# Kernel tuning notes

Measured on AMD Instinct MI355X. Metric: run time of the kernel, lower is better.

Reference implementation:

```python
import jax, jax.numpy as jnp
import numpy as np

N, M, D = 32768, 2048, 32


def setup_inputs() -> dict:
    key = jax.random.key(0)
    k1, k2, k3, k4 = jax.random.split(key, 4)
    inputs = jax.random.normal(k1, (N, D), dtype=jnp.float32)
    # matches torch init: abs(10*randn*0.1 + 0.2)
    gamma = jnp.abs(10.0 * jax.random.normal(k2, (M, D, D), dtype=jnp.float32) * 0.1 + 0.2)
    means = jax.random.normal(k3, (M, D), dtype=jnp.float32)
    weights = jax.random.normal(k4, (M,), dtype=jnp.float32)
    return {"inputs": inputs, "gamma": gamma, "means": means, "weights": weights}


def reference(inputs, gamma, means, weights):
    # cov_m = gamma_m @ gamma_m^T  -> symmetric PSD [M, D, D]
    cov = jnp.einsum('mde,mfe->mdf', gamma, gamma)
    # Quadratic form (x - mu)^T C (x - mu) expanded (C symmetric):
    # x^T C_m x via GEMM on flattened outer products: [N, D*D] @ [D*D, M]
    xx = (inputs[:, :, None] * inputs[:, None, :]).reshape(inputs.shape[0], -1)
    quad_x = xx @ cov.reshape(cov.shape[0], -1).T            # [N, M]
    b = jnp.einsum('mde,me->md', cov, means)                 # C_m mu_m, [M, D]
    cross = inputs @ b.T                                     # x^T C_m mu_m, [N, M]
    const = jnp.einsum('md,md->m', b, means)                 # mu^T C mu, [M]
    D_ij = quad_x - 2.0 * cross + const[None, :]             # [N, M]
    out = jnp.exp(-D_ij) @ weights                           # [N]
    return out[:, None]
```

## Files before the change

### kernel.cpp

```cpp
#include <hip/hip_runtime.h>
#include <math.h>


#define NN 32768
#define MM 2048
#define DDIM 32
#define KSYM 576
#define ROWS 128
#define KSTEPS 18
#define SCREEN 120.0f
#define MCAP 2048
#define FCAP 1000000
#define FBLK 64

typedef __attribute__((ext_vector_type(8))) short short8;
typedef __attribute__((ext_vector_type(4))) float floatx4;

__device__ __forceinline__ unsigned int to_bf16(float f) {
  union { float f; unsigned int u; } x; x.f = f;
  return (x.u + 0x7fffu + ((x.u >> 16) & 1u)) >> 16;
}

struct DFTab { unsigned char d[528]; unsigned char f[528]; };
constexpr DFTab make_df() {
  DFTab t{};
  int s = 0;
  for (int d = 0; d < 32; ++d)
    for (int f = d; f < 32; ++f) {
      t.d[s] = (unsigned char)d; t.f[s] = (unsigned char)f; ++s;
    }
  return t;
}
constexpr DFTab DFT = make_df();

__device__ __forceinline__ float slot_val(const float* v, int s) {
  if (s < 528) return v[DFT.d[s]] * v[DFT.f[s]];
  if (s < 560) return v[s - 528];
  if (s < 562) return 1.f;
  return 0.f;
}

__device__ __forceinline__ void slot_df(int s, int* dd, int* ff) {
  int d = 0, b = 0;
  while (b + (DDIM - d) <= s) { b += DDIM - d; ++d; }
  *dd = d; *ff = d + (s - b);
}

__global__ __launch_bounds__(256) void build_b_kernel(
    const float* __restrict__ gamma, const float* __restrict__ means,
    unsigned short* __restrict__ Bm) {
  __shared__ float G[DDIM][DDIM + 1];
  __shared__ float C[DDIM][DDIM + 1];
  __shared__ float bv[DDIM];
  __shared__ float cc;
  const int m = blockIdx.x;
  const int t = threadIdx.x;
  const float* g = gamma + (size_t)m * DDIM * DDIM;
  for (int l = t; l < DDIM * DDIM; l += 256) G[l >> 5][l & 31] = g[l];
  __syncthreads();
  const float* mu = means + m * DDIM;
  for (int l = t; l < DDIM * DDIM; l += 256) {
    int d = l >> 5, f = l & 31;
    float c = 0.f;
#pragma unroll
    for (int e = 0; e < DDIM; ++e) c += G[d][e] * G[f][e];
    C[d][f] = c;
  }
  __syncthreads();
  if (t < DDIM) {
    float b = 0.f;
#pragma unroll
    for (int f = 0; f < DDIM; ++f) b += C[t][f] * mu[f];
    bv[t] = b;
  }
  __syncthreads();
  if (t == 0) {
    float c = 0.f;
#pragma unroll
    for (int d = 0; d < DDIM; ++d) c += bv[d] * mu[d];
    cc = c;
  }
  __syncthreads();
  unsigned short* brow = Bm + (size_t)m * KSYM;
  for (int s = t; s < KSYM; s += 256) {
    float val;
    if (s < 528) {
      int d, f; slot_df(s, &d, &f);
      val = (d == f) ? C[d][d] : 2.f * C[d][f];
    } else if (s < 560) {
      val = -2.f * bv[s - 528];
    } else if (s == 560) {
      val = cc;
    } else if (s == 561) {
      unsigned int hi = to_bf16(cc);
      union { unsigned int u; float f; } xh; xh.u = hi << 16;
      val = cc - xh.f;
    } else {
      val = 0.f;
    }
    brow[s] = (unsigned short)to_bf16(val);
  }
}

__device__ __noinline__ double survivor_contrib(
    int m, const float* __restrict__ gamma, const float* __restrict__ means,
    const float* __restrict__ weights, const float* __restrict__ xrow) {
  const float* mu = means + m * DDIM;
  float v[DDIM];
#pragma unroll
  for (int d = 0; d < DDIM; ++d) v[d] = xrow[d] - mu[d];
  const float* g = gamma + (size_t)m * DDIM * DDIM;
  float Dex = 0.f;
  for (int e = 0; e < DDIM; ++e) {
    float y = 0.f;
#pragma unroll
    for (int d = 0; d < DDIM; ++d) y += g[d * DDIM + e] * v[d];
    Dex += y * y;
  }
  float e2 = -Dex * 1.44269504088896340736f;
  float kf = floorf(e2);
  float mant = exp2f(e2 - kf);
  return ldexp((double)(weights[m] * mant), (int)kf);
}

__global__ __launch_bounds__(512, 1) void screen_kernel(
    const float* __restrict__ x, const unsigned short* __restrict__ Bm,
    unsigned int* __restrict__ mcnt, unsigned short* __restrict__ mlist,
    unsigned int* __restrict__ flist, unsigned int* __restrict__ fcount) {
  extern __shared__ __align__(16) unsigned short As[];
  const int t = threadIdx.x;
  const int i0 = blockIdx.x * ROWS;
  const int lane = t & 63, w = t >> 6;
  const int lrow = lane & 15, quad = lane >> 4;
  const int rot = blockIdx.x & 31;

  {
    const int r = t >> 2, j = t & 3;
    float v[DDIM];
#pragma unroll
    for (int q = 0; q < 8; ++q)
      *(floatx4*)&v[q * 4] = *(const floatx4*)(x + (size_t)(i0 + r) * DDIM + q * 4);
#pragma unroll
    for (int jj = 0; jj < 4; ++jj) {
      if (j == jj) {
#pragma unroll
        for (int cc = 0; cc < 18; ++cc) {
          const int c = jj * 18 + cc;
          unsigned int uu[4];
#pragma unroll
          for (int q = 0; q < 4; ++q) {
            const int s0 = c * 8 + q * 2;
            uu[q] = to_bf16(slot_val(v, s0)) | (to_bf16(slot_val(v, s0 + 1)) << 16);
          }
          const int cs = (c & ~7) | ((c & 7) ^ (r & 7));
          uint4 o; o.x = uu[0]; o.y = uu[1]; o.z = uu[2]; o.w = uu[3];
          *(uint4*)&As[r * KSYM + cs * 8] = o;
        }
      }
    }
  }
  __syncthreads();

#pragma unroll 1
  for (int g = 0; g < 4; ++g) {
    const int mq = ((g * 8 + w) + rot) & 31;
    const int m0 = mq * 64;
    const unsigned short* bb0 = Bm + (size_t)(m0 +  0 + lrow) * KSYM + quad * 8;
    const unsigned short* bb1 = Bm + (size_t)(m0 + 16 + lrow) * KSYM + quad * 8;
    const unsigned short* bb2 = Bm + (size_t)(m0 + 32 + lrow) * KSYM + quad * 8;
    const unsigned short* bb3 = Bm + (size_t)(m0 + 48 + lrow) * KSYM + quad * 8;

    floatx4 acc[8][4] = {};
#pragma unroll
    for (int kk = 0; kk < KSTEPS; ++kk) {
      short8 bf[4];
      bf[0] = *(const short8*)(bb0 + kk * 32);
      bf[1] = *(const short8*)(bb1 + kk * 32);
      bf[2] = *(const short8*)(bb2 + kk * 32);
      bf[3] = *(const short8*)(bb3 + kk * 32);
      short8 af[8];
#pragma unroll
      for (int ti = 0; ti < 8; ++ti) {
        int rr = ti * 16 + lrow;
        int c = kk * 4 + quad;
        int cs = (c & ~7) | ((c & 7) ^ (rr & 7));
        af[ti] = *(const short8*)&As[rr * KSYM + cs * 8];
      }
#pragma unroll
      for (int ti = 0; ti < 8; ++ti)
#pragma unroll
        for (int mj = 0; mj < 4; ++mj)
          acc[ti][mj] = __builtin_amdgcn_mfma_f32_16x16x32_bf16(
              af[ti], bf[mj], acc[ti][mj], 0, 0, 0);
    }

#pragma unroll
    for (int ti = 0; ti < 8; ++ti)
#pragma unroll
      for (int mj = 0; mj < 4; ++mj)
#pragma unroll
        for (int r = 0; r < 4; ++r) {
          float Dt = acc[ti][mj][r];
          if (Dt < SCREEN) {
            int gi = i0 + ti * 16 + quad * 4 + r;
            int gm = m0 + mj * 16 + lrow;
            unsigned int idx = atomicAdd(&mcnt[gm], 1u);
            if (idx < MCAP) {
              mlist[(size_t)gm * MCAP + idx] = (unsigned short)gi;
            } else {
              unsigned int fi = atomicAdd(fcount, 1u);
              if (fi < FCAP)
                flist[fi] = ((unsigned int)gi << 11) | (unsigned int)gm;
            }
          }
        }
  }
}

__global__ __launch_bounds__(256) void survivor2_kernel(
    const unsigned int* __restrict__ mcnt, const unsigned short* __restrict__ mlist,
    const unsigned int* __restrict__ flist, const unsigned int* __restrict__ fcount,
    const float* __restrict__ x, const float* __restrict__ gamma,
    const float* __restrict__ means, const float* __restrict__ weights,
    double* __restrict__ acc_out) {
  const int blk = blockIdx.x;
  const int t = threadIdx.x;
  if (blk >= MM) {
    unsigned int total = *fcount;
    if (total > FCAP) total = FCAP;
    for (unsigned int idx = (blk - MM) * 256 + t; idx < total; idx += FBLK * 256) {
      unsigned int p = flist[idx];
      int gi = (int)(p >> 11), gm = (int)(p & 2047u);
      double c = survivor_contrib(gm, gamma, means, weights, x + (size_t)gi * DDIM);
      atomicAdd(&acc_out[gi], c);
    }
    return;
  }
  __shared__ float Gt[DDIM][DDIM + 1];
  __shared__ float mu[DDIM];
  const int m = blk;
  unsigned int cnt = mcnt[m];
  if (cnt > MCAP) cnt = MCAP;
  if (cnt == 0) return;
  const float* g = gamma + (size_t)m * DDIM * DDIM;
  for (int l = t; l < DDIM * DDIM; l += 256) Gt[l & 31][l >> 5] = g[l];
  if (t < DDIM) mu[t] = means[m * DDIM + t];
  __syncthreads();
  const float wm = weights[m];
  for (unsigned int s = t; s < cnt; s += 256) {
    int gi = mlist[(size_t)m * MCAP + s];
    float v[DDIM];
#pragma unroll
    for (int q = 0; q < 8; ++q) {
      floatx4 xv = *(const floatx4*)(x + (size_t)gi * DDIM + q * 4);
      v[q * 4 + 0] = xv.x - mu[q * 4 + 0];
      v[q * 4 + 1] = xv.y - mu[q * 4 + 1];
      v[q * 4 + 2] = xv.z - mu[q * 4 + 2];
      v[q * 4 + 3] = xv.w - mu[q * 4 + 3];
    }
    float Dex = 0.f;
#pragma unroll
    for (int e = 0; e < DDIM; ++e) {
      float y = 0.f;
#pragma unroll
      for (int d = 0; d < DDIM; ++d) y += Gt[e][d] * v[d];
      Dex += y * y;
    }
    float e2 = -Dex * 1.44269504088896340736f;
    float kf = floorf(e2);
    float mant = exp2f(e2 - kf);
    atomicAdd(&acc_out[gi], ldexp((double)(wm * mant), (int)kf));
  }
}

__global__ __launch_bounds__(256) void finalize_kernel(
    const double* __restrict__ acc, float* __restrict__ out) {
  int i = blockIdx.x * 256 + threadIdx.x;
  out[i] = (float)acc[i];
}

extern "C" void kernel_launch(void* const* d_in, const int* in_sizes, int n_in,
                              void* d_out, int out_size, void* d_ws, size_t ws_size,
                              hipStream_t stream) {
  (void)in_sizes; (void)n_in; (void)out_size;
  const float* x       = (const float*)d_in[0];
  const float* gamma   = (const float*)d_in[1];
  const float* means   = (const float*)d_in[2];
  const float* weights = (const float*)d_in[3];

  char* p = (char*)d_ws;
  double* acc          = (double*)p;            p += (size_t)NN * 8;
  unsigned int* fcount = (unsigned int*)p;      p += 16;
  unsigned int* mcnt   = (unsigned int*)p;      p += (size_t)MM * 4;
  unsigned short* mlist= (unsigned short*)p;    p += (size_t)MM * MCAP * 2;
  unsigned int* flist  = (unsigned int*)p;      p += (size_t)FCAP * 4;
  unsigned short* Bm   = (unsigned short*)p;    p += (size_t)MM * KSYM * 2;
  const size_t needed = (size_t)(p - (char*)d_ws);
  const size_t zero_bytes = (size_t)NN * 8 + 16 + (size_t)MM * 4;
  if (ws_size < needed) return;

  (void)hipFuncSetAttribute((const void*)screen_kernel,
                            hipFuncAttributeMaxDynamicSharedMemorySize,
                            ROWS * KSYM * 2);

  hipMemsetAsync(d_ws, 0, zero_bytes, stream);
  hipLaunchKernelGGL(build_b_kernel, dim3(MM), dim3(256), 0, stream, gamma, means, Bm);
  hipLaunchKernelGGL(screen_kernel, dim3(NN / ROWS), dim3(512),
                     ROWS * KSYM * 2, stream,
                     x, Bm, mcnt, mlist, flist, fcount);
  hipLaunchKernelGGL(survivor2_kernel, dim3(MM + FBLK), dim3(256), 0, stream,
                     mcnt, mlist, flist, fcount, x, gamma, means, weights, acc);
  hipLaunchKernelGGL(finalize_kernel, dim3(NN / 256), dim3(256), 0, stream,
                     acc, (float*)d_out);
}
```

Measured before the change: 185.1 us.

## Fuse build, screen, survivor and finalize into one cooperative persistent kernel

```diff
diff --git a/kernel.cpp b/kernel.cpp
--- a/kernel.cpp
+++ b/kernel.cpp
@@ -1,5 +1,8 @@
 #include <hip/hip_runtime.h>
+#include <hip/hip_cooperative_groups.h>
 #include <math.h>
+
+namespace cg = cooperative_groups;
 
 
 #define NN 32768
@@ -11,7 +14,8 @@
 #define SCREEN 120.0f
 #define MCAP 2048
 #define FCAP 1000000
-#define FBLK 64
+#define GRID 256
+#define TPB 512
 
 typedef __attribute__((ext_vector_type(8))) short short8;
 typedef __attribute__((ext_vector_type(4))) float floatx4;
@@ -46,62 +50,6 @@
   *dd = d; *ff = d + (s - b);
 }
 
-__global__ __launch_bounds__(256) void build_b_kernel(
-    const float* __restrict__ gamma, const float* __restrict__ means,
-    unsigned short* __restrict__ Bm) {
-  __shared__ float G[DDIM][DDIM + 1];
-  __shared__ float C[DDIM][DDIM + 1];
-  __shared__ float bv[DDIM];
-  __shared__ float cc;
-  const int m = blockIdx.x;
-  const int t = threadIdx.x;
-  const float* g = gamma + (size_t)m * DDIM * DDIM;
-  for (int l = t; l < DDIM * DDIM; l += 256) G[l >> 5][l & 31] = g[l];
-  __syncthreads();
-  const float* mu = means + m * DDIM;
-  for (int l = t; l < DDIM * DDIM; l += 256) {
-    int d = l >> 5, f = l & 31;
-    float c = 0.f;
-#pragma unroll
-    for (int e = 0; e < DDIM; ++e) c += G[d][e] * G[f][e];
-    C[d][f] = c;
-  }
-  __syncthreads();
-  if (t < DDIM) {
-    float b = 0.f;
-#pragma unroll
-    for (int f = 0; f < DDIM; ++f) b += C[t][f] * mu[f];
-    bv[t] = b;
-  }
-  __syncthreads();
-  if (t == 0) {
-    float c = 0.f;
-#pragma unroll
-    for (int d = 0; d < DDIM; ++d) c += bv[d] * mu[d];
-    cc = c;
-  }
-  __syncthreads();
-  unsigned short* brow = Bm + (size_t)m * KSYM;
-  for (int s = t; s < KSYM; s += 256) {
-    float val;
-    if (s < 528) {
-      int d, f; slot_df(s, &d, &f);
-      val = (d == f) ? C[d][d] : 2.f * C[d][f];
-    } else if (s < 560) {
-      val = -2.f * bv[s - 528];
-    } else if (s == 560) {
-      val = cc;
-    } else if (s == 561) {
-      unsigned int hi = to_bf16(cc);
-      union { unsigned int u; float f; } xh; xh.u = hi << 16;
-      val = cc - xh.f;
-    } else {
-      val = 0.f;
-    }
-    brow[s] = (unsigned short)to_bf16(val);
-  }
-}
-
 __device__ __noinline__ double survivor_contrib(
     int m, const float* __restrict__ gamma, const float* __restrict__ means,
     const float* __restrict__ weights, const float* __restrict__ xrow) {
@@ -123,160 +71,232 @@
   return ldexp((double)(weights[m] * mant), (int)kf);
 }
 
-__global__ __launch_bounds__(512, 1) void screen_kernel(
-    const float* __restrict__ x, const unsigned short* __restrict__ Bm,
-    unsigned int* __restrict__ mcnt, unsigned short* __restrict__ mlist,
-    unsigned int* __restrict__ flist, unsigned int* __restrict__ fcount) {
+__global__ __launch_bounds__(TPB, 1) void fused_kernel(
+    const float* __restrict__ x, const float* __restrict__ gamma,
+    const float* __restrict__ means, const float* __restrict__ weights,
+    unsigned short* __restrict__ Bm, unsigned int* __restrict__ mcnt,
+    unsigned short* __restrict__ mlist, unsigned int* __restrict__ flist,
+    unsigned int* __restrict__ fcount, double* __restrict__ acc_g,
+    float* __restrict__ out) {
   extern __shared__ __align__(16) unsigned short As[];
+  cg::grid_group grid = cg::this_grid();
   const int t = threadIdx.x;
-  const int i0 = blockIdx.x * ROWS;
-  const int lane = t & 63, w = t >> 6;
-  const int lrow = lane & 15, quad = lane >> 4;
-  const int rot = blockIdx.x & 31;
+  const int blk = blockIdx.x;
 
   {
-    const int r = t >> 2, j = t & 3;
-    float v[DDIM];
-#pragma unroll
-    for (int q = 0; q < 8; ++q)
-      *(floatx4*)&v[q * 4] = *(const floatx4*)(x + (size_t)(i0 + r) * DDIM + q * 4);
-#pragma unroll
-    for (int jj = 0; jj < 4; ++jj) {
-      if (j == jj) {
-#pragma unroll
-        for (int cc = 0; cc < 18; ++cc) {
-          const int c = jj * 18 + cc;
-          unsigned int uu[4];
-#pragma unroll
-          for (int q = 0; q < 4; ++q) {
-            const int s0 = c * 8 + q * 2;
-            uu[q] = to_bf16(slot_val(v, s0)) | (to_bf16(slot_val(v, s0 + 1)) << 16);
+    if (t < 128) acc_g[blk * 128 + t] = 0.0;
+    if (t >= 128 && t < 136) mcnt[blk * 8 + (t - 128)] = 0u;
+    if (blk == 0 && t == 136) *fcount = 0u;
+  }
+
+  {
+    float* G  = (float*)As;
+    float* C  = G + 32 * 33;
+    float* bv = C + 32 * 33;
+    float* cp = bv + 32;
+#pragma unroll 1
+    for (int mi = 0; mi < 8; ++mi) {
+      const int m = blk * 8 + mi;
+      const float* g = gamma + (size_t)m * DDIM * DDIM;
+      const float* mu = means + m * DDIM;
+      for (int l = t; l < DDIM * DDIM; l += TPB) G[(l >> 5) * 33 + (l & 31)] = g[l];
+      __syncthreads();
+      for (int l = t; l < DDIM * DDIM; l += TPB) {
+        int d = l >> 5, f = l & 31;
+        float c = 0.f;
+#pragma unroll
+        for (int e = 0; e < DDIM; ++e) c += G[d * 33 + e] * G[f * 33 + e];
+        C[d * 33 + f] = c;
+      }
+      __syncthreads();
+      if (t < DDIM) {
+        float b = 0.f;
+#pragma unroll
+        for (int f = 0; f < DDIM; ++f) b += C[t * 33 + f] * mu[f];
+        bv[t] = b;
+      }
+      __syncthreads();
+      if (t == 0) {
+        float c = 0.f;
+#pragma unroll
+        for (int d = 0; d < DDIM; ++d) c += bv[d] * mu[d];
+        *cp = c;
+      }
+      __syncthreads();
+      unsigned short* brow = Bm + (size_t)m * KSYM;
+      const float cc = *cp;
+      for (int s = t; s < KSYM; s += TPB) {
+        float val;
+        if (s < 528) {
+          int d, f; slot_df(s, &d, &f);
+          val = (d == f) ? C[d * 33 + d] : 2.f * C[d * 33 + f];
+        } else if (s < 560) {
+          val = -2.f * bv[s - 528];
+        } else if (s == 560) {
+          val = cc;
+        } else if (s == 561) {
+          unsigned int hi = to_bf16(cc);
+          union { unsigned int u; float f; } xh; xh.u = hi << 16;
+          val = cc - xh.f;
+        } else {
+          val = 0.f;
+        }
+        brow[s] = (unsigned short)to_bf16(val);
+      }
+      __syncthreads();
+    }
+  }
+
+  grid.sync();
+
+  {
+    const int i0 = blk * ROWS;
+    const int lane = t & 63, w = t >> 6;
+    const int lrow = lane & 15, quad = lane >> 4;
+    const int rot = blk & 31;
+
+    {
+      const int r = t >> 2, j = t & 3;
+      float v[DDIM];
+#pragma unroll
+      for (int q = 0; q < 8; ++q)
+        *(floatx4*)&v[q * 4] = *(const floatx4*)(x + (size_t)(i0 + r) * DDIM + q * 4);
+#pragma unroll
+      for (int jj = 0; jj < 4; ++jj) {
+        if (j == jj) {
+#pragma unroll
+          for (int cc2 = 0; cc2 < 18; ++cc2) {
+            const int c = jj * 18 + cc2;
+            unsigned int uu[4];
+#pragma unroll
+            for (int q = 0; q < 4; ++q) {
+              const int s0 = c * 8 + q * 2;
+              uu[q] = to_bf16(slot_val(v, s0)) | (to_bf16(slot_val(v, s0 + 1)) << 16);
+            }
+            const int cs = (c & ~7) | ((c & 7) ^ (r & 7));
+            uint4 o; o.x = uu[0]; o.y = uu[1]; o.z = uu[2]; o.w = uu[3];
+            *(uint4*)&As[r * KSYM + cs * 8] = o;
           }
-          const int cs = (c & ~7) | ((c & 7) ^ (r & 7));
-          uint4 o; o.x = uu[0]; o.y = uu[1]; o.z = uu[2]; o.w = uu[3];
-          *(uint4*)&As[r * KSYM + cs * 8] = o;
         }
       }
     }
-  }
-  __syncthreads();
+    __syncthreads();
 
 #pragma unroll 1
-  for (int g = 0; g < 4; ++g) {
-    const int mq = ((g * 8 + w) + rot) & 31;
-    const int m0 = mq * 64;
-    const unsigned short* bb0 = Bm + (size_t)(m0 +  0 + lrow) * KSYM + quad * 8;
-    const unsigned short* bb1 = Bm + (size_t)(m0 + 16 + lrow) * KSYM + quad * 8;
-    const unsigned short* bb2 = Bm + (size_t)(m0 + 32 + lrow) * KSYM + quad * 8;
-    const unsigned short* bb3 = Bm + (size_t)(m0 + 48 + lrow) * KSYM + quad * 8;
-
-    floatx4 acc[8][4] = {};
-#pragma unroll
-    for (int kk = 0; kk < KSTEPS; ++kk) {
-      short8 bf[4];
-      bf[0] = *(const short8*)(bb0 + kk * 32);
-      bf[1] = *(const short8*)(bb1 + kk * 32);
-      bf[2] = *(const short8*)(bb2 + kk * 32);
-      bf[3] = *(const short8*)(bb3 + kk * 32);
-      short8 af[8];
-#pragma unroll
-      for (int ti = 0; ti < 8; ++ti) {
-        int rr = ti * 16 + lrow;
-        int c = kk * 4 + quad;
-        int cs = (c & ~7) | ((c & 7) ^ (rr & 7));
-        af[ti] = *(const short8*)&As[rr * KSYM + cs * 8];
-      }
+    for (int g = 0; g < 4; ++g) {
+      const int mq = ((g * 8 + w) + rot) & 31;
+      const int m0 = mq * 64;
+      const unsigned short* bb0 = Bm + (size_t)(m0 +  0 + lrow) * KSYM + quad * 8;
+      const unsigned short* bb1 = Bm + (size_t)(m0 + 16 + lrow) * KSYM + quad * 8;
+      const unsigned short* bb2 = Bm + (size_t)(m0 + 32 + lrow) * KSYM + quad * 8;
+      const unsigned short* bb3 = Bm + (size_t)(m0 + 48 + lrow) * KSYM + quad * 8;
+
+      floatx4 acc[8][4] = {};
+#pragma unroll
+      for (int kk = 0; kk < KSTEPS; ++kk) {
+        short8 bf[4];
+        bf[0] = *(const short8*)(bb0 + kk * 32);
+        bf[1] = *(const short8*)(bb1 + kk * 32);
+        bf[2] = *(const short8*)(bb2 + kk * 32);
+        bf[3] = *(const short8*)(bb3 + kk * 32);
+        short8 af[8];
+#pragma unroll
+        for (int ti = 0; ti < 8; ++ti) {
+          int rr = ti * 16 + lrow;
+          int c = kk * 4 + quad;
+          int cs = (c & ~7) | ((c & 7) ^ (rr & 7));
+          af[ti] = *(const short8*)&As[rr * KSYM + cs * 8];
+        }
+#pragma unroll
+        for (int ti = 0; ti < 8; ++ti)
+#pragma unroll
+          for (int mj = 0; mj < 4; ++mj)
+            acc[ti][mj] = __builtin_amdgcn_mfma_f32_16x16x32_bf16(
+                af[ti], bf[mj], acc[ti][mj], 0, 0, 0);
+      }
+
 #pragma unroll
       for (int ti = 0; ti < 8; ++ti)
 #pragma unroll
         for (int mj = 0; mj < 4; ++mj)
-          acc[ti][mj] = __builtin_amdgcn_mfma_f32_16x16x32_bf16(
-              af[ti], bf[mj], acc[ti][mj], 0, 0, 0);
-    }
-
-#pragma unroll
-    for (int ti = 0; ti < 8; ++ti)
-#pragma unroll
-      for (int mj = 0; mj < 4; ++mj)
-#pragma unroll
-        for (int r = 0; r < 4; ++r) {
-          float Dt = acc[ti][mj][r];
-          if (Dt < SCREEN) {
-            int gi = i0 + ti * 16 + quad * 4 + r;
-            int gm = m0 + mj * 16 + lrow;
-            unsigned int idx = atomicAdd(&mcnt[gm], 1u);
-            if (idx < MCAP) {
-              mlist[(size_t)gm * MCAP + idx] = (unsigned short)gi;
-            } else {
-              unsigned int fi = atomicAdd(fcount, 1u);
-              if (fi < FCAP)
-                flist[fi] = ((unsigned int)gi << 11) | (unsigned int)gm;
+#pragma unroll
+          for (int r = 0; r < 4; ++r) {
+            float Dt = acc[ti][mj][r];
+            if (Dt < SCREEN) {
+              int gi = i0 + ti * 16 + quad * 4 + r;
+              int gm = m0 + mj * 16 + lrow;
+              unsigned int idx = atomicAdd(&mcnt[gm], 1u);
+              if (idx < MCAP) {
+                mlist[(size_t)gm * MCAP + idx] = (unsigned short)gi;
+              } else {
+                unsigned int fi = atomicAdd(fcount, 1u);
+                if (fi < FCAP)
+                  flist[fi] = ((unsigned int)gi << 11) | (unsigned int)gm;
+              }
             }
           }
+    }
+  }
+
+  grid.sync();
+
+  {
+    float* Gt = (float*)As;
+    float* mus = Gt + 32 * 33;
+#pragma unroll 1
+    for (int mi = 0; mi < 8; ++mi) {
+      const int m = blk * 8 + mi;
+      unsigned int cnt = mcnt[m];
+      if (cnt > MCAP) cnt = MCAP;
+      if (cnt > 0) {
+        const float* g = gamma + (size_t)m * DDIM * DDIM;
+        for (int l = t; l < DDIM * DDIM; l += TPB) Gt[(l & 31) * 33 + (l >> 5)] = g[l];
+        if (t < DDIM) mus[t] = means[m * DDIM + t];
+        __syncthreads();
+        const float wm = weights[m];
+        for (unsigned int s = t; s < cnt; s += TPB) {
+          int gi = mlist[(size_t)m * MCAP + s];
+          float v[DDIM];
+#pragma unroll
+          for (int q = 0; q < 8; ++q) {
+            floatx4 xv = *(const floatx4*)(x + (size_t)gi * DDIM + q * 4);
+            v[q * 4 + 0] = xv.x - mus[q * 4 + 0];
+            v[q * 4 + 1] = xv.y - mus[q * 4 + 1];
+            v[q * 4 + 2] = xv.z - mus[q * 4 + 2];
+            v[q * 4 + 3] = xv.w - mus[q * 4 + 3];
+          }
+          float Dex = 0.f;
+#pragma unroll
+          for (int e = 0; e < DDIM; ++e) {
+            float y = 0.f;
+#pragma unroll
+            for (int d = 0; d < DDIM; ++d) y += Gt[e * 33 + d] * v[d];
+            Dex += y * y;
+          }
+          float e2 = -Dex * 1.44269504088896340736f;
+          float kf = floorf(e2);
+          float mant = exp2f(e2 - kf);
+          atomicAdd(&acc_g[gi], ldexp((double)(wm * mant), (int)kf));
         }
-  }
-}
-
-__global__ __launch_bounds__(256) void survivor2_kernel(
-    const unsigned int* __restrict__ mcnt, const unsigned short* __restrict__ mlist,
-    const unsigned int* __restrict__ flist, const unsigned int* __restrict__ fcount,
-    const float* __restrict__ x, const float* __restrict__ gamma,
-    const float* __restrict__ means, const float* __restrict__ weights,
-    double* __restrict__ acc_out) {
-  const int blk = blockIdx.x;
-  const int t = threadIdx.x;
-  if (blk >= MM) {
+        __syncthreads();
+      }
+    }
     unsigned int total = *fcount;
     if (total > FCAP) total = FCAP;
-    for (unsigned int idx = (blk - MM) * 256 + t; idx < total; idx += FBLK * 256) {
-      unsigned int p = flist[idx];
-      int gi = (int)(p >> 11), gm = (int)(p & 2047u);
+    for (unsigned int idx = blk * TPB + t; idx < total; idx += GRID * TPB) {
+      unsigned int pck = flist[idx];
+      int gi = (int)(pck >> 11), gm = (int)(pck & 2047u);
       double c = survivor_contrib(gm, gamma, means, weights, x + (size_t)gi * DDIM);
-      atomicAdd(&acc_out[gi], c);
-    }
-    return;
-  }
-  __shared__ float Gt[DDIM][DDIM + 1];
-  __shared__ float mu[DDIM];
-  const int m = blk;
-  unsigned int cnt = mcnt[m];
-  if (cnt > MCAP) cnt = MCAP;
-  if (cnt == 0) return;
-  const float* g = gamma + (size_t)m * DDIM * DDIM;
-  for (int l = t; l < DDIM * DDIM; l += 256) Gt[l & 31][l >> 5] = g[l];
-  if (t < DDIM) mu[t] = means[m * DDIM + t];
-  __syncthreads();
-  const float wm = weights[m];
-  for (unsigned int s = t; s < cnt; s += 256) {
-    int gi = mlist[(size_t)m * MCAP + s];
-    float v[DDIM];
-#pragma unroll
-    for (int q = 0; q < 8; ++q) {
-      floatx4 xv = *(const floatx4*)(x + (size_t)gi * DDIM + q * 4);
-      v[q * 4 + 0] = xv.x - mu[q * 4 + 0];
-      v[q * 4 + 1] = xv.y - mu[q * 4 + 1];
-      v[q * 4 + 2] = xv.z - mu[q * 4 + 2];
-      v[q * 4 + 3] = xv.w - mu[q * 4 + 3];
-    }
-    float Dex = 0.f;
-#pragma unroll
-    for (int e = 0; e < DDIM; ++e) {
-      float y = 0.f;
-#pragma unroll
-      for (int d = 0; d < DDIM; ++d) y += Gt[e][d] * v[d];
-      Dex += y * y;
-    }
-    float e2 = -Dex * 1.44269504088896340736f;
-    float kf = floorf(e2);
-    float mant = exp2f(e2 - kf);
-    atomicAdd(&acc_out[gi], ldexp((double)(wm * mant), (int)kf));
-  }
-}
-
-__global__ __launch_bounds__(256) void finalize_kernel(
-    const double* __restrict__ acc, float* __restrict__ out) {
-  int i = blockIdx.x * 256 + threadIdx.x;
-  out[i] = (float)acc[i];
+      atomicAdd(&acc_g[gi], c);
+    }
+  }
+
+  grid.sync();
+
+  if (t < 128) {
+    int i = blk * 128 + t;
+    out[i] = (float)acc_g[i];
+  }
 }
 
 extern "C" void kernel_launch(void* const* d_in, const int* in_sizes, int n_in,
@@ -287,6 +307,7 @@
   const float* gamma   = (const float*)d_in[1];
   const float* means   = (const float*)d_in[2];
   const float* weights = (const float*)d_in[3];
+  float* outp          = (float*)d_out;
 
   char* p = (char*)d_ws;
   double* acc          = (double*)p;            p += (size_t)NN * 8;
@@ -296,20 +317,15 @@
   unsigned int* flist  = (unsigned int*)p;      p += (size_t)FCAP * 4;
   unsigned short* Bm   = (unsigned short*)p;    p += (size_t)MM * KSYM * 2;
   const size_t needed = (size_t)(p - (char*)d_ws);
-  const size_t zero_bytes = (size_t)NN * 8 + 16 + (size_t)MM * 4;
   if (ws_size < needed) return;
 
-  (void)hipFuncSetAttribute((const void*)screen_kernel,
+  (void)hipFuncSetAttribute((const void*)fused_kernel,
                             hipFuncAttributeMaxDynamicSharedMemorySize,
                             ROWS * KSYM * 2);
 
-  hipMemsetAsync(d_ws, 0, zero_bytes, stream);
-  hipLaunchKernelGGL(build_b_kernel, dim3(MM), dim3(256), 0, stream, gamma, means, Bm);
-  hipLaunchKernelGGL(screen_kernel, dim3(NN / ROWS), dim3(512),
-                     ROWS * KSYM * 2, stream,
-                     x, Bm, mcnt, mlist, flist, fcount);
-  hipLaunchKernelGGL(survivor2_kernel, dim3(MM + FBLK), dim3(256), 0, stream,
-                     mcnt, mlist, flist, fcount, x, gamma, means, weights, acc);
-  hipLaunchKernelGGL(finalize_kernel, dim3(NN / 256), dim3(256), 0, stream,
-                     acc, (float*)d_out);
-}
+  void* args[] = {(void*)&x, (void*)&gamma, (void*)&means, (void*)&weights,
+                  (void*)&Bm, (void*)&mcnt, (void*)&mlist, (void*)&flist,
+                  (void*)&fcount, (void*)&acc, (void*)&outp};
+  hipLaunchCooperativeKernel((const void*)fused_kernel, dim3(GRID), dim3(TPB),
+                             args, ROWS * KSYM * 2, stream);
+}
```

Measured after the change: 348.8 us. +88.4%, slower.
